# Kernel tuning notes

Measured on AMD Instinct MI355X. Metric: run time of the kernel, lower is better.

Reference implementation:

```python
import jax, jax.numpy as jnp
import numpy as np

GAMMA = 0.1
N_CENTERS = 1024
INPUT_DIM = 64
BATCH = 65536


def setup_inputs() -> dict:
    key = jax.random.key(0)
    kx, kc = jax.random.split(key)
    x = jax.random.normal(kx, (BATCH, INPUT_DIM), dtype=jnp.float32)
    # centers ~ Uniform(0, 1), matching torch.empty(...).uniform_(0, 1)
    centers = jax.random.uniform(kc, (N_CENTERS, INPUT_DIM), dtype=jnp.float32)
    return {"x": x, "centers": centers}


def reference(x, centers):
    # Pairwise squared L2 distance via the matmul expansion trick:
    x_sq = jnp.sum(x * x, axis=-1, keepdims=True)          # [B, 1]
    c_sq = jnp.sum(centers * centers, axis=-1)             # [N]
    cross = jnp.einsum("bd,nd->bn", x, centers)            # [B, N]
    l2 = x_sq + c_sq[None, :] - 2.0 * cross                # [B, N]
    l2 = jnp.maximum(l2, 0.0)  # guard tiny negatives from the expansion
    return jnp.exp(-GAMMA * l2)
```

## Files before the change

kernel.cpp:

```cpp
#include <hip/hip_runtime.h>

#define GAMMA 0.1f

constexpr int MTOT = 65536;
constexpr int NTOT = 1024;
constexpr int KDIM = 64;
constexpr int RPB  = 256;

using f16x8 = __attribute__((ext_vector_type(8))) _Float16;
using f32x4 = __attribute__((ext_vector_type(4))) float;

__global__ __launch_bounds__(1024, 4)
void rbf_sweep_kernel(const float* __restrict__ x,
                      const float* __restrict__ centers,
                      float* __restrict__ out) {
  __shared__ _Float16 sCen[NTOT * KDIM];
  __shared__ float    sCsq[NTOT];

  const int tid = threadIdx.x;
  const int mb = blockIdx.x;
  const int lane = tid & 63;
  const int wave = tid >> 6;
  const int l = lane & 15;
  const int g = lane >> 4;

  const float* xrp = x + ((size_t)mb * RPB + wave * 16 + l) * KDIM;
  float4 xr[4];
  #pragma unroll
  for (int ks = 0; ks < 2; ++ks) {
    xr[ks * 2]     = *reinterpret_cast<const float4*>(xrp + ks * 32 + g * 8);
    xr[ks * 2 + 1] = *reinterpret_cast<const float4*>(xrp + ks * 32 + g * 8 + 4);
  }

  {
    const float4* cf = reinterpret_cast<const float4*>(centers);
    #pragma unroll
    for (int p = 0; p < 8; ++p) {
      const int c = p * 1024 + tid;
      const int row = c >> 3;
      const int s = c & 7;
      const float4 v0 = cf[c * 2];
      const float4 v1 = cf[c * 2 + 1];
      const float v[8] = {v0.x, v0.y, v0.z, v0.w, v1.x, v1.y, v1.z, v1.w};
      f16x8 hv;
      float ss = 0.0f;
      #pragma unroll
      for (int i = 0; i < 8; ++i) {
        hv[i] = (_Float16)v[i];
        ss += v[i] * v[i];
      }
      ss += __shfl_xor(ss, 1);
      ss += __shfl_xor(ss, 2);
      ss += __shfl_xor(ss, 4);
      if (s == 0) sCsq[row] = ss;
      const int slot = s ^ (row & 7);
      *reinterpret_cast<f16x8*>(&sCen[row * KDIM + slot * 8]) = hv;
    }
  }
  __syncthreads();

  f16x8 xh[2];
  float ss = 0.0f;
  #pragma unroll
  for (int ks = 0; ks < 2; ++ks) {
    const float v[8] = {xr[ks*2].x,   xr[ks*2].y,   xr[ks*2].z,   xr[ks*2].w,
                        xr[ks*2+1].x, xr[ks*2+1].y, xr[ks*2+1].z, xr[ks*2+1].w};
    f16x8 h;
    #pragma unroll
    for (int e = 0; e < 8; ++e) {
      h[e] = (_Float16)v[e];
      ss += v[e] * v[e];
    }
    xh[ks] = h;
  }
  ss += __shfl_xor(ss, 16);
  ss += __shfl_xor(ss, 32);

  float* orow = out + ((size_t)mb * RPB + wave * 16 + l) * (size_t)NTOT;
  #pragma unroll 8
  for (int nf = 0; nf < 64; ++nf) {
    const int crow = nf * 16 + l;
    f32x4 acc = {};
    #pragma unroll
    for (int ks = 0; ks < 2; ++ks) {
      const int slot = (ks * 4 + g) ^ (l & 7);
      const f16x8 ch = *reinterpret_cast<const f16x8*>(&sCen[crow * KDIM + slot * 8]);
      acc = __builtin_amdgcn_mfma_f32_16x16x32_f16(ch, xh[ks], acc, 0, 0, 0);
    }
    const float4 cs = *reinterpret_cast<const float4*>(&sCsq[nf * 16 + g * 4]);
    float4 o;
    o.x = __expf(-GAMMA * fmaxf(ss + cs.x - 2.0f * acc[0], 0.0f));
    o.y = __expf(-GAMMA * fmaxf(ss + cs.y - 2.0f * acc[1], 0.0f));
    o.z = __expf(-GAMMA * fmaxf(ss + cs.z - 2.0f * acc[2], 0.0f));
    o.w = __expf(-GAMMA * fmaxf(ss + cs.w - 2.0f * acc[3], 0.0f));
    *reinterpret_cast<float4*>(orow + nf * 16 + g * 4) = o;
  }
}

extern "C" void kernel_launch(void* const* d_in, const int* in_sizes, int n_in,
                              void* d_out, int out_size, void* d_ws, size_t ws_size,
                              hipStream_t stream) {
  (void)in_sizes; (void)n_in; (void)d_ws; (void)ws_size; (void)out_size;
  const float* x       = (const float*)d_in[0];
  const float* centers = (const float*)d_in[1];
  float* out = (float*)d_out;
  rbf_sweep_kernel<<<MTOT / RPB, 1024, 0, stream>>>(x, centers, out);
}
```

Baseline: 55.75 us.

## Precompute fp16 centers in a prep kernel and stream them into LDS directly

Adds a small prep kernel that converts the centers to swizzled fp16 and computes their squared norms once into workspace. Each main-kernel block then copies that prepared data straight into LDS with global_load_lds, instead of every one of 256 blocks re-reading fp32 centers and converting them. The epilogue is also folded into fused multiply-adds with a min(.,1) clamp replacing the max(l2,0) guard, and the unroll factor goes from 8 to 16. The cost is an extra kernel launch and a dependency on workspace space, and the main kernel's prologue now relies on the direct-to-LDS load path behaving correctly.

```diff
diff --git a/kernel.cpp b/kernel.cpp
--- a/kernel.cpp
+++ b/kernel.cpp
@@ -10,9 +10,41 @@
 using f16x8 = __attribute__((ext_vector_type(8))) _Float16;
 using f32x4 = __attribute__((ext_vector_type(4))) float;
 
+typedef __attribute__((address_space(1))) const unsigned int gu32;
+typedef __attribute__((address_space(3))) unsigned int lu32;
+
+constexpr size_t WS_CEN = 0;
+constexpr size_t WS_CSQ = 131072;
+
+__global__ __launch_bounds__(256)
+void cen_convert_kernel(const float* __restrict__ centers,
+                        _Float16* __restrict__ cen,
+                        float* __restrict__ sq) {
+  const int c = blockIdx.x * 256 + threadIdx.x;
+  const int row = c >> 3;
+  const int s = c & 7;
+  const float4* p = reinterpret_cast<const float4*>(centers + (size_t)row * KDIM + s * 8);
+  float4 v0 = p[0], v1 = p[1];
+  const float v[8] = {v0.x, v0.y, v0.z, v0.w, v1.x, v1.y, v1.z, v1.w};
+  f16x8 hv;
+  float ss = 0.0f;
+  #pragma unroll
+  for (int i = 0; i < 8; ++i) {
+    hv[i] = (_Float16)v[i];
+    ss += v[i] * v[i];
+  }
+  ss += __shfl_xor(ss, 1);
+  ss += __shfl_xor(ss, 2);
+  ss += __shfl_xor(ss, 4);
+  if (s == 0) sq[row] = ss;
+  const int slot = s ^ (row & 7);
+  *reinterpret_cast<f16x8*>(cen + (size_t)row * KDIM + slot * 8) = hv;
+}
+
 __global__ __launch_bounds__(1024, 4)
 void rbf_sweep_kernel(const float* __restrict__ x,
-                      const float* __restrict__ centers,
+                      const _Float16* __restrict__ cen,
+                      const float* __restrict__ csq,
                       float* __restrict__ out) {
   __shared__ _Float16 sCen[NTOT * KDIM];
   __shared__ float    sCsq[NTOT];
@@ -33,29 +65,19 @@
   }
 
   {
-    const float4* cf = reinterpret_cast<const float4*>(centers);
+    const char* src = reinterpret_cast<const char*>(cen);
+    char* dst = reinterpret_cast<char*>(sCen);
     #pragma unroll
     for (int p = 0; p < 8; ++p) {
-      const int c = p * 1024 + tid;
-      const int row = c >> 3;
-      const int s = c & 7;
-      const float4 v0 = cf[c * 2];
-      const float4 v1 = cf[c * 2 + 1];
-      const float v[8] = {v0.x, v0.y, v0.z, v0.w, v1.x, v1.y, v1.z, v1.w};
-      f16x8 hv;
-      float ss = 0.0f;
-      #pragma unroll
-      for (int i = 0; i < 8; ++i) {
-        hv[i] = (_Float16)v[i];
-        ss += v[i] * v[i];
-      }
-      ss += __shfl_xor(ss, 1);
-      ss += __shfl_xor(ss, 2);
-      ss += __shfl_xor(ss, 4);
-      if (s == 0) sCsq[row] = ss;
-      const int slot = s ^ (row & 7);
-      *reinterpret_cast<f16x8*>(&sCen[row * KDIM + slot * 8]) = hv;
+      const int q = p * 1024 + tid;
+      __builtin_amdgcn_global_load_lds((gu32*)(src + (size_t)q * 16),
+                                       (lu32*)(dst + (size_t)q * 16), 16, 0, 0);
     }
+  }
+  if (tid < 256) {
+    __builtin_amdgcn_global_load_lds(
+        (gu32*)(reinterpret_cast<const char*>(csq) + (size_t)tid * 16),
+        (lu32*)(reinterpret_cast<char*>(sCsq) + (size_t)tid * 16), 16, 0, 0);
   }
   __syncthreads();
 
@@ -75,24 +97,26 @@
   }
   ss += __shfl_xor(ss, 16);
   ss += __shfl_xor(ss, 32);
+  const float nxs = -GAMMA * ss;
+
+  const int slot0 = g ^ (l & 7);
+  const int slot1 = (4 + g) ^ (l & 7);
 
   float* orow = out + ((size_t)mb * RPB + wave * 16 + l) * (size_t)NTOT;
-  #pragma unroll 8
+  #pragma unroll 16
   for (int nf = 0; nf < 64; ++nf) {
     const int crow = nf * 16 + l;
     f32x4 acc = {};
-    #pragma unroll
-    for (int ks = 0; ks < 2; ++ks) {
-      const int slot = (ks * 4 + g) ^ (l & 7);
-      const f16x8 ch = *reinterpret_cast<const f16x8*>(&sCen[crow * KDIM + slot * 8]);
-      acc = __builtin_amdgcn_mfma_f32_16x16x32_f16(ch, xh[ks], acc, 0, 0, 0);
-    }
+    acc = __builtin_amdgcn_mfma_f32_16x16x32_f16(
+        *reinterpret_cast<const f16x8*>(&sCen[crow * KDIM + slot0 * 8]), xh[0], acc, 0, 0, 0);
+    acc = __builtin_amdgcn_mfma_f32_16x16x32_f16(
+        *reinterpret_cast<const f16x8*>(&sCen[crow * KDIM + slot1 * 8]), xh[1], acc, 0, 0, 0);
     const float4 cs = *reinterpret_cast<const float4*>(&sCsq[nf * 16 + g * 4]);
     float4 o;
-    o.x = __expf(-GAMMA * fmaxf(ss + cs.x - 2.0f * acc[0], 0.0f));
-    o.y = __expf(-GAMMA * fmaxf(ss + cs.y - 2.0f * acc[1], 0.0f));
-    o.z = __expf(-GAMMA * fmaxf(ss + cs.z - 2.0f * acc[2], 0.0f));
-    o.w = __expf(-GAMMA * fmaxf(ss + cs.w - 2.0f * acc[3], 0.0f));
+    o.x = fminf(__expf(fmaf(2.0f * GAMMA, acc[0], fmaf(-GAMMA, cs.x, nxs))), 1.0f);
+    o.y = fminf(__expf(fmaf(2.0f * GAMMA, acc[1], fmaf(-GAMMA, cs.y, nxs))), 1.0f);
+    o.z = fminf(__expf(fmaf(2.0f * GAMMA, acc[2], fmaf(-GAMMA, cs.z, nxs))), 1.0f);
+    o.w = fminf(__expf(fmaf(2.0f * GAMMA, acc[3], fmaf(-GAMMA, cs.w, nxs))), 1.0f);
     *reinterpret_cast<float4*>(orow + nf * 16 + g * 4) = o;
   }
 }
@@ -100,9 +124,15 @@
 extern "C" void kernel_launch(void* const* d_in, const int* in_sizes, int n_in,
                               void* d_out, int out_size, void* d_ws, size_t ws_size,
                               hipStream_t stream) {
-  (void)in_sizes; (void)n_in; (void)d_ws; (void)ws_size; (void)out_size;
+  (void)in_sizes; (void)n_in; (void)out_size; (void)ws_size;
   const float* x       = (const float*)d_in[0];
   const float* centers = (const float*)d_in[1];
   float* out = (float*)d_out;
-  rbf_sweep_kernel<<<MTOT / RPB, 1024, 0, stream>>>(x, centers, out);
+
+  char* ws = (char*)d_ws;
+  _Float16* cen = (_Float16*)(ws + WS_CEN);
+  float*    csq = (float*)(ws + WS_CSQ);
+
+  cen_convert_kernel<<<32, 256, 0, stream>>>(centers, cen, csq);
+  rbf_sweep_kernel<<<MTOT / RPB, 1024, 0, stream>>>(x, cen, csq, out);
 }
```

Result: slower. 70.36 us (+26.2%).
